# Kernel optimization log

Hardware: AMD Instinct MI355X
Metric: run time of the kernel (lower is better)

## Reference

```python
import jax, jax.numpy as jnp
import numpy as np

N_NODES = 100000
N_EDGES = 1600000
IN_F = 256
OUT_F = 128


def setup_inputs() -> dict:
    key = jax.random.key(0)
    k1, k2, k3, k4, k5, k6 = jax.random.split(key, 6)
    x = jax.random.normal(k1, (N_NODES, IN_F), dtype=jnp.float32)
    edge_row = jax.random.randint(k2, (N_EDGES,), 0, N_NODES)  # destination (output row)
    edge_col = jax.random.randint(k3, (N_EDGES,), 0, N_NODES)  # source (gathered node)
    edge_val = jax.random.uniform(k4, (N_EDGES,), dtype=jnp.float32)  # normalized adj weights
    # Xavier-uniform init like nn.init.xavier_uniform_
    limit = float(np.sqrt(6.0 / (IN_F + OUT_F)))
    weight = jax.random.uniform(k5, (IN_F, OUT_F), dtype=jnp.float32, minval=-limit, maxval=limit)
    bias = jnp.zeros((OUT_F,), dtype=jnp.float32)
    return {"x": x, "edge_row": edge_row, "edge_col": edge_col,
            "edge_val": edge_val, "weight": weight, "bias": bias}


def reference(x, edge_row, edge_col, edge_val, weight, bias):
    # Dense transform: h = x @ W + b   -> [N, OUT_F]
    h = x @ weight + bias
    # Sparse adjacency matmul: out[i] = sum_{e: row[e]==i} val[e] * h[col[e]]
    msg = h[edge_col] * edge_val[:, None]  # [E, OUT_F] gather + scale
    out = jax.ops.segment_sum(msg, edge_row, num_segments=N_NODES)
    return out
```

## Files before the change

### kernel.cpp

```cpp
#include <hip/hip_runtime.h>

#define IN_F 256
#define OUT_F 128
#define CAP 5120
#define EPB 8192

typedef __attribute__((ext_vector_type(8))) short short8;
typedef __attribute__((ext_vector_type(4))) float floatx4;
typedef __attribute__((ext_vector_type(2))) float floatx2;

__device__ __forceinline__ unsigned short f2bf(float f) {
    union { float f; unsigned int u; } v; v.f = f;
    unsigned int u = v.u;
    unsigned int r = (u + 0x7FFFu + ((u >> 16) & 1u)) >> 16;
    return (unsigned short)r;
}

__global__ __launch_bounds__(256) void prep_kernel(
    const float* __restrict__ w, unsigned short* __restrict__ w_t,
    int* __restrict__ cursor, int nb)
{
    const int g = blockIdx.x * 256 + threadIdx.x;
    if (g < IN_F * OUT_F) {
        const int n = g >> 8;
        const int k = g & 255;
        w_t[n * 256 + k] = f2bf(w[k * OUT_F + n]);
    }
    if (g < nb) cursor[g] = 0;
}

#define XS2 264
#define HS2 136
#define GEMM_SMEM 33792

__device__ __forceinline__ void gemm_body(
    char* smem,
    const float* __restrict__ x, const unsigned short* __restrict__ w_t,
    const float* __restrict__ bias, unsigned short* __restrict__ h_bf,
    int tile, int M)
{
    unsigned short* xs = (unsigned short*)smem;

    const int tid  = threadIdx.x;
    const int w    = tid >> 6;
    const int l    = tid & 63;
    const int m16  = l & 15;
    const int g    = l >> 4;
    const int row0 = tile * 64;

    short8 bf[2][8];
    #pragma unroll
    for (int nt = 0; nt < 2; nt++)
        #pragma unroll
        for (int ks = 0; ks < 8; ks++)
            bf[nt][ks] = *(const short8*)(
                w_t + (w * 32 + nt * 16 + m16) * 256 + ks * 32 + g * 8);

    #pragma unroll
    for (int s = 0; s < 16; s++) {
        const int idx = tid + s * 256;
        const int row = idx >> 6;
        const int c4  = idx & 63;
        const int gr  = row0 + row;
        float4 v = make_float4(0.f, 0.f, 0.f, 0.f);
        if (gr < M) v = *(const float4*)(x + (size_t)gr * IN_F + c4 * 4);
        ushort4 b;
        b.x = f2bf(v.x); b.y = f2bf(v.y); b.z = f2bf(v.z); b.w = f2bf(v.w);
        *(ushort4*)(xs + row * XS2 + c4 * 4) = b;
    }
    __syncthreads();

    floatx4 acc[4][2];
    #pragma unroll
    for (int mt = 0; mt < 4; mt++) {
        acc[mt][0] = (floatx4){0.f, 0.f, 0.f, 0.f};
        acc[mt][1] = (floatx4){0.f, 0.f, 0.f, 0.f};
    }

    #pragma unroll
    for (int ks = 0; ks < 8; ks++) {
        #pragma unroll
        for (int mt = 0; mt < 4; mt++) {
            const short8 a = *(const short8*)(xs + (mt * 16 + m16) * XS2 + ks * 32 + g * 8);
            acc[mt][0] = __builtin_amdgcn_mfma_f32_16x16x32_bf16(a, bf[0][ks], acc[mt][0], 0, 0, 0);
            acc[mt][1] = __builtin_amdgcn_mfma_f32_16x16x32_bf16(a, bf[1][ks], acc[mt][1], 0, 0, 0);
        }
    }
    __syncthreads();

    unsigned short* hs = xs;
    #pragma unroll
    for (int nt = 0; nt < 2; nt++) {
        const int col = w * 32 + nt * 16 + m16;
        const float bv = bias[col];
        #pragma unroll
        for (int mt = 0; mt < 4; mt++)
            #pragma unroll
            for (int r = 0; r < 4; r++)
                hs[(mt * 16 + g * 4 + r) * HS2 + col] = f2bf(acc[mt][nt][r] + bv);
    }
    __syncthreads();

    {
        const int row = tid >> 2;
        const int seg = tid & 3;
        const int gr  = row0 + row;
        if (gr < M) {
            #pragma unroll
            for (int q = 0; q < 4; q++) {
                const uint4 v = *(const uint4*)(hs + row * HS2 + seg * 32 + q * 8);
                *(uint4*)(h_bf + (size_t)gr * OUT_F + seg * 32 + q * 8) = v;
            }
        }
    }
}

__device__ __forceinline__ void sort_body(
    char* smem, const int* __restrict__ erow, const int* __restrict__ ecol,
    const float* __restrict__ eval, int* __restrict__ cursor,
    uint2* __restrict__ tmp, int E, int nb, int blk)
{
    int* lcnt  = (int*)smem;
    int* lbase = lcnt + 512;
    for (int i = threadIdx.x; i < nb; i += 256) lcnt[i] = 0;
    __syncthreads();
    const int base = blk * EPB;

    unsigned int rec[EPB / 256];
    #pragma unroll
    for (int i = 0; i < EPB / 256; i++) {
        const int e = base + i * 256 + threadIdx.x;
        rec[i] = 0xFFFFFFFFu;
        if (e < E) {
            const int r = erow[e];
            const int b = r >> 8;
            const int lp = atomicAdd(&lcnt[b], 1);
            rec[i] = ((unsigned int)lp << 17) | ((unsigned int)(r & 255) << 9)
                   | (unsigned int)b;
        }
    }
    __syncthreads();

    for (int i = threadIdx.x; i < nb; i += 256) {
        const int c = lcnt[i];
        lbase[i] = c ? atomicAdd(&cursor[i], c) : 0;
    }
    __syncthreads();

    #pragma unroll
    for (int i = 0; i < EPB / 256; i++) {
        if (rec[i] != 0xFFFFFFFFu) {
            const int e  = base + i * 256 + threadIdx.x;
            const int b  = rec[i] & 511;
            const int rl = (rec[i] >> 9) & 255;
            const int lp = rec[i] >> 17;
            const int pos = lbase[b] + lp;
            if (pos < CAP)
                tmp[(size_t)b * CAP + pos] = make_uint2(
                    ((unsigned int)rl << 24) | (unsigned int)ecol[e],
                    __float_as_uint(eval[e]));
        }
    }
}

__device__ __forceinline__ void csr_body(
    char* smem, uint2* __restrict__ tmp, const int* __restrict__ cursor,
    int* __restrict__ start, int* __restrict__ endx, int M, int blk)
{
    int* nh   = (int*)smem;
    int* nst  = nh + 256;
    int* ncur = nst + 256;
    unsigned int* lcv = (unsigned int*)(smem + 3072);

    const int b  = blk;
    const size_t tb = (size_t)b * CAP;
    const int cnt = min(cursor[b], CAP);
    const int t  = threadIdx.x;

    nh[t] = 0;
    __syncthreads();
    for (int i = t; i < cnt; i += 256) atomicAdd(&nh[tmp[tb + i].x >> 24], 1);
    __syncthreads();

    const int v = nh[t];
    nst[t] = v;
    __syncthreads();
    for (int off = 1; off < 256; off <<= 1) {
        const int u = (t >= off) ? nst[t - off] : 0;
        __syncthreads();
        nst[t] += u;
        __syncthreads();
    }
    const int ex = nst[t] - v;
    const int node = b * 256 + t;
    const int cvbase = b * CAP * 2;
    if (node < M) { start[node] = cvbase + ex; endx[node] = cvbase + ex + v; }
    ncur[t] = ex;
    __syncthreads();

    for (int i = t; i < cnt; i += 256) {
        const uint2 p = tmp[tb + i];
        const int d  = p.x >> 24;
        const int lp = atomicAdd(&ncur[d], 1);
        const float f = __uint_as_float(p.y);
        const int q = min((int)(f * 32768.0f), 32767);
        lcv[lp] = ((p.x & 0x00FFFFFFu) << 15) | (unsigned int)q;
    }
    __syncthreads();

    unsigned int* cvp = (unsigned int*)tmp;
    for (int i = t; i < cnt; i += 256) cvp[(size_t)cvbase + i] = lcv[i];
}

__global__ __launch_bounds__(256) void k_sort_gemm(
    const int* __restrict__ erow, const int* __restrict__ ecol,
    const float* __restrict__ eval, int* __restrict__ cursor,
    uint2* __restrict__ tmp, int E, int nb, int EB,
    const float* __restrict__ x, const unsigned short* __restrict__ w_t,
    const float* __restrict__ bias, unsigned short* __restrict__ h_bf,
    int M, int tile0)
{
    __shared__ __align__(16) char smem[GEMM_SMEM];
    if ((int)blockIdx.x < EB)
        sort_body(smem, erow, ecol, eval, cursor, tmp, E, nb, blockIdx.x);
    else
        gemm_body(smem, x, w_t, bias, h_bf, tile0 + (int)blockIdx.x - EB, M);
}

__global__ __launch_bounds__(256) void k_csr_gemm(
    uint2* __restrict__ tmp, const int* __restrict__ cursor,
    int* __restrict__ start, int* __restrict__ endx, int nb,
    const float* __restrict__ x, const unsigned short* __restrict__ w_t,
    const float* __restrict__ bias, unsigned short* __restrict__ h_bf,
    int M, int tile0)
{
    __shared__ __align__(16) char smem[GEMM_SMEM];
    if ((int)blockIdx.x < nb)
        csr_body(smem, tmp, cursor, start, endx, M, blockIdx.x);
    else
        gemm_body(smem, x, w_t, bias, h_bf, tile0 + (int)blockIdx.x - nb, M);
}

__global__ __launch_bounds__(256) void gather_kernel(
    const unsigned short* __restrict__ h_bf, const int* __restrict__ start,
    const int* __restrict__ endx, const unsigned int* __restrict__ cv,
    float* __restrict__ out, int N)
{
    const int node = (blockIdx.x * 256 + threadIdx.x) >> 6;
    const int lane = threadIdx.x & 63;
    if (node >= N) return;

    const int s   = start[node];
    const int end = endx[node];
    const unsigned int* hp = (const unsigned int*)h_bf;

    float acc0 = 0.f, acc1 = 0.f;
    int j = s;
    for (; j + 16 <= end; j += 16) {
        unsigned int mu[16];
        #pragma unroll
        for (int u = 0; u < 16; u++)
            mu[u] = __builtin_amdgcn_readfirstlane(
                __builtin_nontemporal_load(cv + j + u));
        unsigned int p[16];
        #pragma unroll
        for (int u = 0; u < 16; u++)
            p[u] = *(hp + (size_t)(mu[u] >> 15) * 64 + lane);
        #pragma unroll
        for (int u = 0; u < 16; u++) {
            const float v = (float)(mu[u] & 0x7FFFu) * (1.0f / 32768.0f) + (0.5f / 32768.0f);
            acc0 += v * __uint_as_float(p[u] << 16);
            acc1 += v * __uint_as_float(p[u] & 0xFFFF0000u);
        }
    }
    for (; j + 8 <= end; j += 8) {
        unsigned int mu[8];
        #pragma unroll
        for (int u = 0; u < 8; u++)
            mu[u] = __builtin_amdgcn_readfirstlane(
                __builtin_nontemporal_load(cv + j + u));
        unsigned int p[8];
        #pragma unroll
        for (int u = 0; u < 8; u++)
            p[u] = *(hp + (size_t)(mu[u] >> 15) * 64 + lane);
        #pragma unroll
        for (int u = 0; u < 8; u++) {
            const float v = (float)(mu[u] & 0x7FFFu) * (1.0f / 32768.0f) + (0.5f / 32768.0f);
            acc0 += v * __uint_as_float(p[u] << 16);
            acc1 += v * __uint_as_float(p[u] & 0xFFFF0000u);
        }
    }
    for (; j < end; j++) {
        const unsigned int mu = __builtin_amdgcn_readfirstlane(
            __builtin_nontemporal_load(cv + j));
        const unsigned int p = *(hp + (size_t)(mu >> 15) * 64 + lane);
        const float v = (float)(mu & 0x7FFFu) * (1.0f / 32768.0f) + (0.5f / 32768.0f);
        acc0 += v * __uint_as_float(p << 16);
        acc1 += v * __uint_as_float(p & 0xFFFF0000u);
    }
    floatx2 o; o.x = acc0; o.y = acc1;
    __builtin_nontemporal_store(o, (floatx2*)(out + (size_t)node * OUT_F + lane * 2));
}

extern "C" void kernel_launch(void* const* d_in, const int* in_sizes, int n_in,
                              void* d_out, int out_size, void* d_ws, size_t ws_size,
                              hipStream_t stream) {
    const float* x     = (const float*)d_in[0];
    const int*   erow  = (const int*)d_in[1];
    const int*   ecol  = (const int*)d_in[2];
    const float* eval  = (const float*)d_in[3];
    const float* wgt   = (const float*)d_in[4];
    const float* bias  = (const float*)d_in[5];
    float*       out   = (float*)d_out;

    const int M  = in_sizes[0] / IN_F;
    const int E  = in_sizes[1];
    const int nb = (M + 255) >> 8;
    const int EB = (E + EPB - 1) / EPB;
    const int GT = (M + 63) / 64;
    const int S1 = (GT * 45) / 100;
    const int S2 = GT - S1;

    char* ws = (char*)d_ws;
    unsigned short* h_bf = (unsigned short*)ws;  ws += (size_t)M * OUT_F * 2;
    unsigned short* w_t  = (unsigned short*)ws;  ws += (size_t)IN_F * OUT_F * 2;
    int* cursor      = (int*)ws;                 ws += ((size_t)nb * 4 + 15) & ~15ull;
    int* start       = (int*)ws;                 ws += ((size_t)M * 4 + 15) & ~15ull;
    int* endx        = (int*)ws;                 ws += ((size_t)M * 4 + 15) & ~15ull;
    uint2* tmp       = (uint2*)ws;               ws += (size_t)nb * CAP * 8;
    unsigned int* cv = (unsigned int*)tmp;

    prep_kernel<<<(IN_F * OUT_F + 255) / 256, 256, 0, stream>>>(wgt, w_t, cursor, nb);

    k_sort_gemm<<<EB + S1, 256, 0, stream>>>(erow, ecol, eval, cursor, tmp, E, nb, EB,
                                             x, w_t, bias, h_bf, M, 0);

    k_csr_gemm<<<nb + S2, 256, 0, stream>>>(tmp, cursor, start, endx, nb,
                                            x, w_t, bias, h_bf, M, S1);

    const long long work = (long long)M * 64;
    gather_kernel<<<(int)((work + 255) / 256), 256, 0, stream>>>(
        h_bf, start, endx, cv, out, M);
}
```

Measured before the change: 323.6 us.

## Fuse CSR build and gather into one kernel using LDS-resident edge lists

Merges the per-bucket CSR construction and the gather into a single 1024-thread kernel. Each block sorts its bucket's edges into LDS and then gathers directly from LDS, so the compressed edge list and the start/end arrays are no longer written to and re-read from global memory. The GEMM is moved entirely into the sort kernel, which drops the split of GEMM tiles across two launches. In exchange, the gather now runs with only nb blocks (one per 256 nodes), which lowers gather parallelism, and the GEMM no longer overlaps the CSR phase.

```diff
diff --git a/kernel.cpp b/kernel.cpp
--- a/kernel.cpp
+++ b/kernel.cpp
@@ -163,42 +163,55 @@
     }
 }
 
-__device__ __forceinline__ void csr_body(
-    char* smem, uint2* __restrict__ tmp, const int* __restrict__ cursor,
-    int* __restrict__ start, int* __restrict__ endx, int M, int blk)
-{
-    int* nh   = (int*)smem;
-    int* nst  = nh + 256;
-    int* ncur = nst + 256;
-    unsigned int* lcv = (unsigned int*)(smem + 3072);
-
-    const int b  = blk;
+__global__ __launch_bounds__(256) void k_sort_gemm(
+    const int* __restrict__ erow, const int* __restrict__ ecol,
+    const float* __restrict__ eval, int* __restrict__ cursor,
+    uint2* __restrict__ tmp, int E, int nb, int EB,
+    const float* __restrict__ x, const unsigned short* __restrict__ w_t,
+    const float* __restrict__ bias, unsigned short* __restrict__ h_bf, int M)
+{
+    __shared__ __align__(16) char smem[GEMM_SMEM];
+    if ((int)blockIdx.x < EB)
+        sort_body(smem, erow, ecol, eval, cursor, tmp, E, nb, blockIdx.x);
+    else
+        gemm_body(smem, x, w_t, bias, h_bf, (int)blockIdx.x - EB, M);
+}
+
+__global__ __launch_bounds__(1024, 8) void k_csrgather(
+    const uint2* __restrict__ tmp, const int* __restrict__ cursor,
+    const unsigned short* __restrict__ h_bf, float* __restrict__ out, int M)
+{
+    __shared__ int nh[256], nst[256], ncur[256];
+    __shared__ unsigned int lcv[CAP];
+
+    const int b  = blockIdx.x;
     const size_t tb = (size_t)b * CAP;
     const int cnt = min(cursor[b], CAP);
     const int t  = threadIdx.x;
 
-    nh[t] = 0;
-    __syncthreads();
-    for (int i = t; i < cnt; i += 256) atomicAdd(&nh[tmp[tb + i].x >> 24], 1);
-    __syncthreads();
-
-    const int v = nh[t];
-    nst[t] = v;
+    if (t < 256) nh[t] = 0;
+    __syncthreads();
+    for (int i = t; i < cnt; i += 1024) atomicAdd(&nh[tmp[tb + i].x >> 24], 1);
+    __syncthreads();
+
+    int v = 0;
+    if (t < 256) { v = nh[t]; nst[t] = v; }
     __syncthreads();
     for (int off = 1; off < 256; off <<= 1) {
-        const int u = (t >= off) ? nst[t - off] : 0;
+        int u = 0;
+        if (t < 256 && t >= off) u = nst[t - off];
         __syncthreads();
-        nst[t] += u;
+        if (t < 256) nst[t] += u;
         __syncthreads();
     }
-    const int ex = nst[t] - v;
-    const int node = b * 256 + t;
-    const int cvbase = b * CAP * 2;
-    if (node < M) { start[node] = cvbase + ex; endx[node] = cvbase + ex + v; }
-    ncur[t] = ex;
-    __syncthreads();
-
-    for (int i = t; i < cnt; i += 256) {
+    if (t < 256) {
+        const int ex = nst[t] - v;
+        nst[t]  = ex;
+        ncur[t] = ex;
+    }
+    __syncthreads();
+
+    for (int i = t; i < cnt; i += 1024) {
         const uint2 p = tmp[tb + i];
         const int d  = p.x >> 24;
         const int lp = atomicAdd(&ncur[d], 1);
@@ -208,98 +221,44 @@
     }
     __syncthreads();
 
-    unsigned int* cvp = (unsigned int*)tmp;
-    for (int i = t; i < cnt; i += 256) cvp[(size_t)cvbase + i] = lcv[i];
-}
-
-__global__ __launch_bounds__(256) void k_sort_gemm(
-    const int* __restrict__ erow, const int* __restrict__ ecol,
-    const float* __restrict__ eval, int* __restrict__ cursor,
-    uint2* __restrict__ tmp, int E, int nb, int EB,
-    const float* __restrict__ x, const unsigned short* __restrict__ w_t,
-    const float* __restrict__ bias, unsigned short* __restrict__ h_bf,
-    int M, int tile0)
-{
-    __shared__ __align__(16) char smem[GEMM_SMEM];
-    if ((int)blockIdx.x < EB)
-        sort_body(smem, erow, ecol, eval, cursor, tmp, E, nb, blockIdx.x);
-    else
-        gemm_body(smem, x, w_t, bias, h_bf, tile0 + (int)blockIdx.x - EB, M);
-}
-
-__global__ __launch_bounds__(256) void k_csr_gemm(
-    uint2* __restrict__ tmp, const int* __restrict__ cursor,
-    int* __restrict__ start, int* __restrict__ endx, int nb,
-    const float* __restrict__ x, const unsigned short* __restrict__ w_t,
-    const float* __restrict__ bias, unsigned short* __restrict__ h_bf,
-    int M, int tile0)
-{
-    __shared__ __align__(16) char smem[GEMM_SMEM];
-    if ((int)blockIdx.x < nb)
-        csr_body(smem, tmp, cursor, start, endx, M, blockIdx.x);
-    else
-        gemm_body(smem, x, w_t, bias, h_bf, tile0 + (int)blockIdx.x - nb, M);
-}
-
-__global__ __launch_bounds__(256) void gather_kernel(
-    const unsigned short* __restrict__ h_bf, const int* __restrict__ start,
-    const int* __restrict__ endx, const unsigned int* __restrict__ cv,
-    float* __restrict__ out, int N)
-{
-    const int node = (blockIdx.x * 256 + threadIdx.x) >> 6;
-    const int lane = threadIdx.x & 63;
-    if (node >= N) return;
-
-    const int s   = start[node];
-    const int end = endx[node];
+    const int wv   = t >> 6;
+    const int lane = t & 63;
     const unsigned int* hp = (const unsigned int*)h_bf;
 
-    float acc0 = 0.f, acc1 = 0.f;
-    int j = s;
-    for (; j + 16 <= end; j += 16) {
-        unsigned int mu[16];
-        #pragma unroll
-        for (int u = 0; u < 16; u++)
-            mu[u] = __builtin_amdgcn_readfirstlane(
-                __builtin_nontemporal_load(cv + j + u));
-        unsigned int p[16];
-        #pragma unroll
-        for (int u = 0; u < 16; u++)
-            p[u] = *(hp + (size_t)(mu[u] >> 15) * 64 + lane);
-        #pragma unroll
-        for (int u = 0; u < 16; u++) {
-            const float v = (float)(mu[u] & 0x7FFFu) * (1.0f / 32768.0f) + (0.5f / 32768.0f);
-            acc0 += v * __uint_as_float(p[u] << 16);
-            acc1 += v * __uint_as_float(p[u] & 0xFFFF0000u);
-        }
-    }
-    for (; j + 8 <= end; j += 8) {
-        unsigned int mu[8];
-        #pragma unroll
-        for (int u = 0; u < 8; u++)
-            mu[u] = __builtin_amdgcn_readfirstlane(
-                __builtin_nontemporal_load(cv + j + u));
-        unsigned int p[8];
-        #pragma unroll
-        for (int u = 0; u < 8; u++)
-            p[u] = *(hp + (size_t)(mu[u] >> 15) * 64 + lane);
-        #pragma unroll
-        for (int u = 0; u < 8; u++) {
-            const float v = (float)(mu[u] & 0x7FFFu) * (1.0f / 32768.0f) + (0.5f / 32768.0f);
-            acc0 += v * __uint_as_float(p[u] << 16);
-            acc1 += v * __uint_as_float(p[u] & 0xFFFF0000u);
-        }
-    }
-    for (; j < end; j++) {
-        const unsigned int mu = __builtin_amdgcn_readfirstlane(
-            __builtin_nontemporal_load(cv + j));
-        const unsigned int p = *(hp + (size_t)(mu >> 15) * 64 + lane);
-        const float v = (float)(mu & 0x7FFFu) * (1.0f / 32768.0f) + (0.5f / 32768.0f);
-        acc0 += v * __uint_as_float(p << 16);
-        acc1 += v * __uint_as_float(p & 0xFFFF0000u);
-    }
-    floatx2 o; o.x = acc0; o.y = acc1;
-    __builtin_nontemporal_store(o, (floatx2*)(out + (size_t)node * OUT_F + lane * 2));
+    for (int k = 0; k < 16; k++) {
+        const int nl   = wv + k * 16;
+        const int node = b * 256 + nl;
+        if (node >= M) continue;
+        const int s = nst[nl];
+        const int e = ncur[nl];
+        float acc0 = 0.f, acc1 = 0.f;
+        int j = s;
+        for (; j + 8 <= e; j += 8) {
+            unsigned int mu[8];
+            #pragma unroll
+            for (int u = 0; u < 8; u++)
+                mu[u] = __builtin_amdgcn_readfirstlane(lcv[j + u]);
+            unsigned int p[8];
+            #pragma unroll
+            for (int u = 0; u < 8; u++)
+                p[u] = hp[(size_t)(mu[u] >> 15) * 64 + lane];
+            #pragma unroll
+            for (int u = 0; u < 8; u++) {
+                const float vv = (float)(mu[u] & 0x7FFFu) * (1.0f / 32768.0f) + (0.5f / 32768.0f);
+                acc0 += vv * __uint_as_float(p[u] << 16);
+                acc1 += vv * __uint_as_float(p[u] & 0xFFFF0000u);
+            }
+        }
+        for (; j < e; j++) {
+            const unsigned int mu = __builtin_amdgcn_readfirstlane(lcv[j]);
+            const unsigned int p = hp[(size_t)(mu >> 15) * 64 + lane];
+            const float vv = (float)(mu & 0x7FFFu) * (1.0f / 32768.0f) + (0.5f / 32768.0f);
+            acc0 += vv * __uint_as_float(p << 16);
+            acc1 += vv * __uint_as_float(p & 0xFFFF0000u);
+        }
+        floatx2 o; o.x = acc0; o.y = acc1;
+        *(floatx2*)(out + (size_t)node * OUT_F + lane * 2) = o;
+    }
 }
 
 extern "C" void kernel_launch(void* const* d_in, const int* in_sizes, int n_in,
@@ -318,27 +277,17 @@
     const int nb = (M + 255) >> 8;
     const int EB = (E + EPB - 1) / EPB;
     const int GT = (M + 63) / 64;
-    const int S1 = (GT * 45) / 100;
-    const int S2 = GT - S1;
 
     char* ws = (char*)d_ws;
     unsigned short* h_bf = (unsigned short*)ws;  ws += (size_t)M * OUT_F * 2;
     unsigned short* w_t  = (unsigned short*)ws;  ws += (size_t)IN_F * OUT_F * 2;
     int* cursor      = (int*)ws;                 ws += ((size_t)nb * 4 + 15) & ~15ull;
-    int* start       = (int*)ws;                 ws += ((size_t)M * 4 + 15) & ~15ull;
-    int* endx        = (int*)ws;                 ws += ((size_t)M * 4 + 15) & ~15ull;
     uint2* tmp       = (uint2*)ws;               ws += (size_t)nb * CAP * 8;
-    unsigned int* cv = (unsigned int*)tmp;
 
     prep_kernel<<<(IN_F * OUT_F + 255) / 256, 256, 0, stream>>>(wgt, w_t, cursor, nb);
 
-    k_sort_gemm<<<EB + S1, 256, 0, stream>>>(erow, ecol, eval, cursor, tmp, E, nb, EB,
-                                             x, w_t, bias, h_bf, M, 0);
-
-    k_csr_gemm<<<nb + S2, 256, 0, stream>>>(tmp, cursor, start, endx, nb,
-                                            x, w_t, bias, h_bf, M, S1);
-
-    const long long work = (long long)M * 64;
-    gather_kernel<<<(int)((work + 255) / 256), 256, 0, stream>>>(
-        h_bf, start, endx, cv, out, M);
-}
+    k_sort_gemm<<<EB + GT, 256, 0, stream>>>(erow, ecol, eval, cursor, tmp, E, nb, EB,
+                                             x, w_t, bias, h_bf, M);
+
+    k_csrgather<<<nb, 1024, 0, stream>>>(tmp, cursor, h_bf, out, M);
+}
```

Result: faster. 283.7 us (-12.4%).
